# Performance work log

Measured on AMD Instinct MI355X. Metric: run time of the kernel, lower is better.

The kernel has to match this reference:

```python
import jax, jax.numpy as jnp
import numpy as np

B, N, E, ATT, TT, IT = 32, 5000, 500, 50, 4, 24
TEMP = 0.5

def leaky(x):
    return jnp.where(x > 0, x, 0.1 * x)

def ln(x, g, b, eps=1e-5):
    m = jnp.mean(x, axis=-1, keepdims=True)
    v = jnp.mean((x - m) ** 2, axis=-1, keepdims=True)
    return (x - m) * jax.lax.rsqrt(v + eps) * g + b

def setup_inputs() -> dict:
    key = jax.random.key(0)
    ks = jax.random.split(key, 16)
    s = 0.05
    return {
        'positive_sample': jax.random.randint(ks[0], (B, 3), 0, N),
        'ent_text_emb': jax.random.normal(ks[1], (N, TT, 384), jnp.float32),
        'ent_img_emb': jax.random.normal(ks[2], (N, IT, 383), jnp.float32),
        'entity_embedding': jax.random.normal(ks[3], (N, E), jnp.float32) * s,
        'relation_embedding': jax.random.normal(ks[4], (N, E), jnp.float32) * s,
        'W_text': jax.random.normal(ks[5], (ATT, 384), jnp.float32) * s,
        'b_text': jnp.zeros((ATT,), jnp.float32),
        'W_img': jax.random.normal(ks[6], (ATT, 383), jnp.float32) * s,
        'b_img': jnp.zeros((ATT,), jnp.float32),
        'W_tproj': jax.random.normal(ks[7], (ATT, ATT * IT), jnp.float32) * s,
        'b_tproj': jnp.zeros((ATT,), jnp.float32),
        'W_iproj': jax.random.normal(ks[8], (ATT, ATT * TT), jnp.float32) * s,
        'b_iproj': jnp.zeros((ATT,), jnp.float32),
        'W_rel1': jax.random.normal(ks[9], (IT * TT, E), jnp.float32) * s,
        'b_rel1': jnp.zeros((IT * TT,), jnp.float32),
        'W_rel2': jax.random.normal(ks[10], (IT * TT, E), jnp.float32) * s,
        'b_rel2': jnp.zeros((IT * TT,), jnp.float32),
        'W1': jax.random.normal(ks[11], (100, 2 * E), jnp.float32) * s,
        'b1': jnp.zeros((100,), jnp.float32),
        'W3': jax.random.normal(ks[12], (E, 100), jnp.float32) * s,
        'b3': jnp.zeros((E,), jnp.float32),
        'ln_g': jnp.ones((ATT,), jnp.float32),
        'ln_b': jnp.zeros((ATT,), jnp.float32),
    }

def _cos_sim(X, p):
    # X [B,N,d], p [B,d]; denominators are detached as in the torch code
    num = jnp.einsum('bnd,bd->bn', X, p)
    den = jnp.linalg.norm(X, axis=2) * jnp.linalg.norm(p, axis=1)[:, None]
    return num / (jax.lax.stop_gradient(den) + 1e-10)

def reference(positive_sample, ent_text_emb, ent_img_emb, entity_embedding,
              relation_embedding, W_text, b_text, W_img, b_img, W_tproj, b_tproj,
              W_iproj, b_iproj, W_rel1, b_rel1, W_rel2, b_rel2, W1, b1, W3, b3,
              ln_g, ln_b):
    rel = relation_embedding[positive_sample[:, 1]]              # [B,E]
    text_emb = leaky(jnp.einsum('ntf,df->ntd', ent_text_emb, W_text) + b_text)  # [N,4,50]
    img_emb = leaky(jnp.einsum('nif,df->nid', ent_img_emb, W_img) + b_img)      # [N,24,50]
    cross = jnp.einsum('nid,ntd->nit', img_emb, text_emb)        # [N,24,4]

    # image branch: softmax over img tokens, plus relation-gated path
    img_att = jnp.einsum('nti,nid->ntd', jax.nn.softmax(cross.transpose(0, 2, 1), axis=2), img_emb)  # [N,4,50]
    rg_i = jax.nn.sigmoid(rel @ W_rel1.T + b_rel1).reshape(B, IT, TT)           # [B,24,4]
    gated_i = rg_i[:, None] * cross[None]                                        # [B,N,24,4]
    img_att_rg = jnp.einsum('bnit,nid->bntd', gated_i, img_emb)                  # [B,N,4,50]
    img_att_all = ln(img_att_rg, ln_g, ln_b) + ln(img_att, ln_g, ln_b)[None]
    img_att_all = img_att_all.reshape(B, N, TT * ATT) @ W_iproj.T + b_iproj      # [B,N,50]

    # text branch: softmax over text tokens, plus relation-gated path
    text_att = jnp.einsum('nit,ntd->nid', jax.nn.softmax(cross, axis=2), text_emb)  # [N,24,50]
    rg_t = jax.nn.sigmoid(rel @ W_rel2.T + b_rel2).reshape(B, IT, TT)
    gated_t = rg_t[:, None] * cross[None]                                        # [B,N,24,4]
    text_att_rg = jnp.einsum('bnit,ntd->bnid', gated_t, text_emb)                # [B,N,24,50]
    text_att_all = ln(text_att_rg, ln_g, ln_b) + ln(text_att, ln_g, ln_b)[None]
    text_att_all = text_att_all.reshape(B, N, IT * ATT) @ W_tproj.T + b_tproj    # [B,N,50]

    # structural gate on KGE entity embeddings (split W1 to avoid concat)
    h = leaky(entity_embedding @ W1[:, :E].T[None].squeeze(0).T.T  # placeholder removed below
              ) if False else None
    h = leaky((entity_embedding @ W1[:, :E].T)[None] + (rel @ W1[:, E:].T)[:, None] + b1)  # [B,N,100]
    gate = jax.nn.sigmoid(h @ W3.T + b3)                                         # [B,N,E]
    t_att = entity_embedding[None] * gate                                        # [B,N,E]

    pos_idx = positive_sample[:, 2]  # tail-batch
    bi = jnp.arange(B)
    pos_img = img_att_all[bi, pos_idx]    # [B,50]
    pos_text = text_att_all[bi, pos_idx]  # [B,50]
    pos_t = t_att[bi, pos_idx]            # [B,E]

    simil_img = _cos_sim(img_att_all, pos_img)
    simil_text = _cos_sim(text_att_all, pos_text)
    simil_t = _cos_sim(t_att, pos_t)

    out = (jax.nn.softmax(simil_t / TEMP, axis=1)
           + jax.nn.softmax(simil_img / TEMP, axis=1)
           + jax.nn.softmax(simil_text / TEMP, axis=1))
    return (out, simil_img, simil_text, simil_t)
```

## Files before the change

### kernel.cpp

```cpp
#include <hip/hip_runtime.h>
#include <math.h>

#define BB 32
#define NN 5000
#define EE 500
#define AT 50
#define TTT 4
#define ITT 24
#define FT 384
#define FI 383
#define KH 100
#define BN (BB*NN)

__device__ __forceinline__ float leaky(float x){ return x > 0.f ? x : 0.1f*x; }
__device__ __forceinline__ float sigm(float x){ return 1.f/(1.f+__expf(-x)); }

enum : size_t {
  O_WTT = 0,
  O_WIT = 19968,
  O_WIP = 39936,
  O_WTP = 50336,
  O_W1T = 112736,
  O_W3T = 162736,
  O_SIP = 212736,
  O_STP = 212944,
  O_CBI = 214192,
  O_CBT = 214244,
  O_RGI = 214296,
  O_RGT = 217368,
  O_RB  = 220440,
  O_A   = 223640,
  O_PT  = 723640,
  O_PTN = 739640,
  O_PIM = 739672,
  O_PIMN= 741336,
  O_PTX = 741368,
  O_PTXN= 743032,
  O_MR  = 743064,
  O_SR  = 743160,
  O_EMB = 743256,
};

__global__ void k_prep(const float* Wt, const float* Wi, const float* Wip, const float* Wtp,
                       const float* W1, const float* W3, const float* g, const float* lb,
                       const float* bip, const float* btp, float* ws){
  (void)W1;
  int id = blockIdx.x*256 + threadIdx.x;
  if (id < 19968){ int f=id/52, d=id%52; ws[O_WTT+id] = (d<50)? Wt[d*FT+f] : 0.f; return; }
  id -= 19968;
  if (id < 19968){ int f=id/52, d=id%52; ws[O_WIT+id] = (f<383 && d<50)? Wi[d*FI+f] : 0.f; return; }
  id -= 19968;
  if (id < 10400){
    int m=id>>2, c=id&3; int d=m%50, r=m/50; int q=r%13, t=r/13; int o=q*4+c;
    ws[O_WIP+id] = (o<50)? Wip[o*200+t*50+d]*g[o] : 0.f; return; }
  id -= 10400;
  if (id < 62400){
    int m=id>>2, c=id&3; int d=m%50, r=m/50; int q=r%13, i=r/13; int o=q*4+c;
    ws[O_WTP+id] = (o<50)? Wtp[o*1200+i*50+d]*g[o] : 0.f; return; }
  id -= 62400;
  if (id < 50000){ int k=id/500, e=id%500; ws[O_W3T+id] = W3[e*100+k]; return; }
  id -= 50000;
  if (id < 208){ int t=id/52, o=id%52; float s=0;
                 if (o<50) for(int d=0;d<50;d++) s += Wip[o*200+t*50+d]*g[d];
                 ws[O_SIP+id]=s; return; }
  id -= 208;
  if (id < 1248){ int i=id/52, o=id%52; float s=0;
                  if (o<50) for(int d=0;d<50;d++) s += Wtp[o*1200+i*50+d]*g[d];
                  ws[O_STP+id]=s; return; }
  id -= 1248;
  if (id < 52){ int o=id; float s=0;
                if (o<50){ for(int j=0;j<200;j++) s += lb[j%50]*Wip[o*200+j]; s=2.f*s+bip[o]; }
                ws[O_CBI+o]=s; return; }
  id -= 52;
  if (id < 52){ int o=id; float s=0;
                if (o<50){ for(int j=0;j<1200;j++) s += lb[j%50]*Wtp[o*1200+j]; s=2.f*s+btp[o]; }
                ws[O_CBT+o]=s; return; }
}

__global__ void k_rel(const int* ps, const float* rele, const float* Wr1, const float* br1,
                      const float* Wr2, const float* br2, const float* W1, float* ws){
  __shared__ float relL[EE];
  int b = blockIdx.x;
  int r = ps[b*3+1];
  for (int e=threadIdx.x; e<EE; e+=256) relL[e] = rele[(size_t)r*EE+e];
  __syncthreads();
  for (int j=threadIdx.x; j<292; j+=256){
    if (j<96){
      float a=br1[j]; const float* w=&Wr1[j*EE];
      for(int e=0;e<EE;e++) a+=relL[e]*w[e];
      ws[O_RGI+b*96+j]=sigm(a);
    } else if (j<192){
      int jj=j-96; float a=br2[jj]; const float* w=&Wr2[jj*EE];
      for(int e=0;e<EE;e++) a+=relL[e]*w[e];
      ws[O_RGT+b*96+jj]=sigm(a);
    } else {
      int k=j-192; float a=0; const float* w=&W1[k*1000+500];
      for(int e=0;e<EE;e++) a+=relL[e]*w[e];
      ws[O_RB+b*100+k]=a;
    }
  }
}

__global__ void k_A(const float* ent, const float* W1, float* ws){
  __shared__ __align__(16) float entL[8*EE];
  int n0 = blockIdx.x*8;
  for (int idx=threadIdx.x; idx<1000; idx+=256)
    *(float4*)&entL[idx*4] = *(const float4*)&ent[(size_t)n0*EE + idx*4];
  __syncthreads();
  for (int idx=threadIdx.x; idx<800; idx+=256){
    int k=idx>>3, rr=idx&7;
    const float4* el=(const float4*)&entL[rr*EE];
    const float4* wr=(const float4*)&W1[(size_t)k*1000];
    float s=0;
    for (int e4=0;e4<125;e4++){
      float4 a=el[e4], w=wr[e4];
      s += a.x*w.x + a.y*w.y + a.z*w.z + a.w*w.w;
    }
    ws[O_A + (size_t)k*NN + (n0+rr)] = s;
  }
}

__global__ void k_pos(const int* ps, const float* ent, const float* b1, const float* b3, float* ws){
  __shared__ float hL[KH];
  __shared__ float red[4];
  int b=blockIdx.x; int n=ps[b*3+2]; int tid=threadIdx.x;
  if (tid<KH) hL[tid] = leaky(ws[O_A+(size_t)tid*NN+n] + ws[O_RB+b*100+tid] + b1[tid]);
  __syncthreads();
  const float* w3t=&ws[O_W3T];
  float sq=0;
  for (int e=tid; e<EE; e+=256){
    float a=b3[e];
    for (int k=0;k<KH;k++) a += hL[k]*w3t[k*500+e];
    float gg=sigm(a); float ta=ent[(size_t)n*EE+e]*gg;
    ws[O_PT+b*500+e]=ta; sq+=ta*ta;
  }
  for (int off=1; off<64; off<<=1) sq += __shfl_xor(sq, off);
  if ((tid&63)==0) red[tid>>6]=sq;
  __syncthreads();
  if (tid==0) ws[O_PTN+b] = sqrtf(red[0]+red[1]+red[2]+red[3]);
}

__global__ __launch_bounds__(256) void k_emb(const float* X, const float* Wp, const float* bias,
                                             float* emb, int R, int F, int rowsPerN, int rowOff,
                                             int xstride){
  __shared__ __align__(16) float Wl[128*52];
  int row0 = blockIdx.x*512 + threadIdx.x;
  int row1 = row0 + 256;
  bool act0 = row0 < R, act1 = row1 < R;
  float4 acc0[13], acc1[13];
  #pragma unroll
  for (int c=0;c<13;c++){ acc0[c]=make_float4(0,0,0,0); acc1[c]=make_float4(0,0,0,0); }
  const float* xr0 = X + (size_t)(act0?row0:0)*xstride;
  const float* xr1 = X + (size_t)(act1?row1:0)*xstride;
  for (int f0=0; f0<F; f0+=128){
    int nf = min(128, F-f0);
    __syncthreads();
    for (int j=threadIdx.x; j<nf*52; j+=256) Wl[j] = Wp[(size_t)f0*52 + j];
    __syncthreads();
    for (int f=0; f<nf; ++f){
      float x0 = xr0[f0+f], x1 = xr1[f0+f];
      const float4* wr = (const float4*)&Wl[f*52];
      #pragma unroll
      for (int c=0;c<13;++c){
        float4 w=wr[c];
        acc0[c].x+=x0*w.x; acc0[c].y+=x0*w.y; acc0[c].z+=x0*w.z; acc0[c].w+=x0*w.w;
        acc1[c].x+=x1*w.x; acc1[c].y+=x1*w.y; acc1[c].z+=x1*w.z; acc1[c].w+=x1*w.w;
      }
    }
  }
  if (act0){
    int n = row0 / rowsPerN, rr = row0 % rowsPerN;
    float* dst = emb + (size_t)n*1456 + (size_t)(rowOff+rr)*52;
    #pragma unroll
    for (int c=0;c<13;++c){
      float4 v=acc0[c]; int o=c*4;
      v.x=leaky(v.x+bias[o]); v.y=leaky(v.y+bias[o+1]);
      if (c<12){ v.z=leaky(v.z+bias[o+2]); v.w=leaky(v.w+bias[o+3]); }
      else { v.z=0.f; v.w=0.f; }
      *(float4*)&dst[o]=v;
    }
  }
  if (act1){
    int n = row1 / rowsPerN, rr = row1 % rowsPerN;
    float* dst = emb + (size_t)n*1456 + (size_t)(rowOff+rr)*52;
    #pragma unroll
    for (int c=0;c<13;++c){
      float4 v=acc1[c]; int o=c*4;
      v.x=leaky(v.x+bias[o]); v.y=leaky(v.y+bias[o+1]);
      if (c<12){ v.z=leaky(v.z+bias[o+2]); v.w=leaky(v.w+bias[o+3]); }
      else { v.z=0.f; v.w=0.f; }
      *(float4*)&dst[o]=v;
    }
  }
}

__global__ __launch_bounds__(256) void k_main(const int* ps, float* ws, float* out, int mode){
  __shared__ __align__(16) float teie[1456];
  __shared__ __align__(16) float Pm[120*52];
  __shared__ __align__(16) float Um[120*32];
  __shared__ __align__(16) float Gi[576];
  __shared__ __align__(16) float crs[96];
  __shared__ __align__(16) float aimg[96], atxt[96];
  __shared__ __align__(16) float part1[96], part2[96];
  __shared__ __align__(16) float aU[120];
  __shared__ float Gts[16], mimg[24], mtxt[4];
  __shared__ float muA1[4], muA2[24];
  __shared__ float accD1[32], accN1[32], accD2[32], accN2[32];

  int tid = threadIdx.x;
  int bstar = blockIdx.x;
  int n = mode ? ps[bstar*3+2] : blockIdx.x;

  const float* embn = &ws[O_EMB + (size_t)n*1456];
  for (int j=tid; j<364; j+=256) *(float4*)&teie[j*4] = *(const float4*)&embn[j*4];
  if (tid<32){ accD1[tid]=0.f; accN1[tid]=0.f; accD2[tid]=0.f; accN2[tid]=0.f; }
  __syncthreads();

  for (int it=tid; it<716; it+=256){
    if (it<576){
      int i=it/24, j=it%24;
      const float4* a=(const float4*)&teie[(4+i)*52];
      const float4* b=(const float4*)&teie[(4+j)*52];
      float s=0;
      #pragma unroll
      for(int d=0;d<13;d++){ float4 x=a[d], y=b[d]; s+=x.x*y.x+x.y*y.y+x.z*y.z+x.w*y.w; }
      Gi[it]=s;
    } else if (it<672){
      int c=it-576; int i=c>>2, t=c&3;
      const float4* a=(const float4*)&teie[(4+i)*52];
      const float4* b=(const float4*)&teie[t*52];
      float s=0;
      #pragma unroll
      for(int d=0;d<13;d++){ float4 x=a[d], y=b[d]; s+=x.x*y.x+x.y*y.y+x.z*y.z+x.w*y.w; }
      crs[c]=s;
    } else if (it<688){
      int c=it-672; int t=c>>2, u=c&3;
      const float4* a=(const float4*)&teie[t*52];
      const float4* b=(const float4*)&teie[u*52];
      float s=0;
      #pragma unroll
      for(int d=0;d<13;d++){ float4 x=a[d], y=b[d]; s+=x.x*y.x+x.y*y.y+x.z*y.z+x.w*y.w; }
      Gts[c]=s;
    } else if (it<712){
      int i=it-688;
      const float4* a=(const float4*)&teie[(4+i)*52];
      float s=0;
      #pragma unroll
      for(int d=0;d<13;d++){ float4 x=a[d]; s+=x.x+x.y+x.z+x.w; }
      mimg[i]=s*0.02f;
    } else {
      int t=it-712;
      const float4* a=(const float4*)&teie[t*52];
      float s=0;
      #pragma unroll
      for(int d=0;d<13;d++){ float4 x=a[d]; s+=x.x+x.y+x.z+x.w; }
      mtxt[t]=s*0.02f;
    }
  }
  __syncthreads();

  if (tid<4){
    int t=tid;
    float mx=-1e30f; for(int i=0;i<24;i++) mx=fmaxf(mx,crs[i*4+t]);
    float ex[24]; float s=0;
    for(int i=0;i<24;i++){ ex[i]=__expf(crs[i*4+t]-mx); s+=ex[i]; }
    float inv=1.f/s; float mu=0;
    for(int i=0;i<24;i++){ float a=ex[i]*inv; aimg[i*4+t]=a; mu+=a*mimg[i]; }
    muA1[t]=mu;
  } else if (tid>=64 && tid<88){
    int i=tid-64;
    float mx=-1e30f; for(int t=0;t<4;t++) mx=fmaxf(mx,crs[i*4+t]);
    float ex[4]; float s=0;
    for(int t=0;t<4;t++){ ex[t]=__expf(crs[i*4+t]-mx); s+=ex[t]; }
    float inv=1.f/s; float mu=0;
    for(int t=0;t<4;t++){ float a=ex[t]*inv; atxt[i*4+t]=a; mu+=a*mtxt[t]; }
    muA2[i]=mu;
  }
  __syncthreads();

  if (tid<208){
    int ig=tid&3, r=tid>>2, q=r%13, t=r/13;
    const float* wb = &ws[O_WIP + (size_t)(t*13+q)*200];
    const float* eb = &teie[(4+ig*6)*52];
    float4 acc[6];
    #pragma unroll
    for (int l=0;l<6;l++) acc[l]=make_float4(0,0,0,0);
    for (int dc=0; dc<12; ++dc){
      float e[6][4];
      #pragma unroll
      for (int l=0;l<6;l++){
        float4 v=*(const float4*)&eb[l*52+dc*4];
        e[l][0]=v.x; e[l][1]=v.y; e[l][2]=v.z; e[l][3]=v.w;
      }
      #pragma unroll
      for (int dd=0; dd<4; ++dd){
        float4 w=*(const float4*)&wb[(dc*4+dd)*4];
        #pragma unroll
        for (int l=0;l<6;l++){
          acc[l].x+=e[l][dd]*w.x; acc[l].y+=e[l][dd]*w.y;
          acc[l].z+=e[l][dd]*w.z; acc[l].w+=e[l][dd]*w.w;
        }
      }
    }
    #pragma unroll
    for (int d=48; d<50; ++d){
      float4 w=*(const float4*)&wb[d*4];
      #pragma unroll
      for (int l=0;l<6;l++){
        float ee=eb[l*52+d];
        acc[l].x+=ee*w.x; acc[l].y+=ee*w.y; acc[l].z+=ee*w.z; acc[l].w+=ee*w.w;
      }
    }
    #pragma unroll
    for (int l=0;l<6;l++) *(float4*)&Pm[(t*24+ig*6+l)*52 + q*4]=acc[l];
  } else {
    for (int c=tid-208; c<244; c+=48){
      if (c<96){
        int i=c>>2, t=c&3;
        float s=0; for(int j=0;j<24;j++) s+=Gi[i*24+j]*aimg[j*4+t];
        part1[c]=aimg[c]*s;
      } else if (c<192){
        int cc=c-96; int t=cc&3;
        float s=0; for(int u=0;u<4;u++) s+=Gts[t*4+u]*atxt[(cc&~3)+u];
        part2[cc]=atxt[cc]*s;
      } else {
        int j=c-192;
        *(float4*)&Pm[96*52+j*4] = *(const float4*)&ws[O_SIP+j*4];
      }
    }
  }
  __syncthreads();

  if (tid<128){
    int b=tid&31, t=tid>>5;
    float w1r[24];
    #pragma unroll
    for(int i=0;i<24;i++) w1r[i]=ws[O_RGI+b*96+i*4+t]*crs[i*4+t];
    float mu=0;
    #pragma unroll
    for(int i=0;i<24;i++) mu+=w1r[i]*mimg[i];
    float q=0;
    #pragma unroll
    for(int i=0;i<24;i++){
      const float4* gr=(const float4*)&Gi[i*24];
      float s=0;
      #pragma unroll
      for(int j4=0;j4<6;j4++){
        float4 g=gr[j4];
        s+=g.x*w1r[j4*4]+g.y*w1r[j4*4+1]+g.z*w1r[j4*4+2]+g.w*w1r[j4*4+3];
      }
      q+=w1r[i]*s;
    }
    float inv=rsqrtf(q*0.02f-mu*mu+1e-5f);
    #pragma unroll
    for(int i=0;i<24;i++) Um[(t*24+i)*32+b]=inv*w1r[i];
    Um[(96+t)*32+b]=-inv*mu;
  } else if (tid<228){
    int z=tid-128;
    int t=(z<96)? (z/24) : (z-96);
    float q=0; for(int i=0;i<24;i++) q+=part1[i*4+t];
    float inv=rsqrtf(q*0.02f-muA1[t]*muA1[t]+1e-5f);
    aU[z]=(z<96)? inv*aimg[(z%24)*4+t] : -inv*muA1[t];
  }
  __syncthreads();

  if (tid<104){
    int bg=tid/13, q=tid-bg*13;
    float4 a0=make_float4(0,0,0,0), a1=make_float4(0,0,0,0);
    float4 a2=make_float4(0,0,0,0), a3=make_float4(0,0,0,0);
    for (int z=0; z<100; ++z){
      float az=aU[z];
      float4 u=*(const float4*)&Um[z*32+bg*4];
      float4 p=*(const float4*)&Pm[z*52+q*4];
      float u0=u.x+az, u1=u.y+az, u2=u.z+az, u3=u.w+az;
      a0.x+=u0*p.x; a0.y+=u0*p.y; a0.z+=u0*p.z; a0.w+=u0*p.w;
      a1.x+=u1*p.x; a1.y+=u1*p.y; a1.z+=u1*p.z; a1.w+=u1*p.w;
      a2.x+=u2*p.x; a2.y+=u2*p.y; a2.z+=u2*p.z; a2.w+=u2*p.w;
      a3.x+=u3*p.x; a3.y+=u3*p.y; a3.z+=u3*p.z; a3.w+=u3*p.w;
    }
    float4 cb=*(const float4*)&ws[O_CBI+q*4];
    a0.x+=cb.x; a0.y+=cb.y; a0.z+=cb.z; a0.w+=cb.w;
    a1.x+=cb.x; a1.y+=cb.y; a1.z+=cb.z; a1.w+=cb.w;
    a2.x+=cb.x; a2.y+=cb.y; a2.z+=cb.z; a2.w+=cb.w;
    a3.x+=cb.x; a3.y+=cb.y; a3.z+=cb.z; a3.w+=cb.w;
    float n0=a0.x*a0.x+a0.y*a0.y+a0.z*a0.z+a0.w*a0.w;
    float n1=a1.x*a1.x+a1.y*a1.y+a1.z*a1.z+a1.w*a1.w;
    float n2=a2.x*a2.x+a2.y*a2.y+a2.z*a2.z+a2.w*a2.w;
    float n3=a3.x*a3.x+a3.y*a3.y+a3.z*a3.z+a3.w*a3.w;
    int b0=bg*4;
    if (!mode){
      const float* PV=&ws[O_PIM];
      float4 p0=*(const float4*)&PV[(b0+0)*52+q*4];
      float4 p1=*(const float4*)&PV[(b0+1)*52+q*4];
      float4 p2=*(const float4*)&PV[(b0+2)*52+q*4];
      float4 p3=*(const float4*)&PV[(b0+3)*52+q*4];
      atomicAdd(&accD1[b0+0], a0.x*p0.x+a0.y*p0.y+a0.z*p0.z+a0.w*p0.w);
      atomicAdd(&accD1[b0+1], a1.x*p1.x+a1.y*p1.y+a1.z*p1.z+a1.w*p1.w);
      atomicAdd(&accD1[b0+2], a2.x*p2.x+a2.y*p2.y+a2.z*p2.z+a2.w*p2.w);
      atomicAdd(&accD1[b0+3], a3.x*p3.x+a3.y*p3.y+a3.z*p3.z+a3.w*p3.w);
      atomicAdd(&accN1[b0+0],n0); atomicAdd(&accN1[b0+1],n1);
      atomicAdd(&accN1[b0+2],n2); atomicAdd(&accN1[b0+3],n3);
    } else {
      atomicAdd(&accN1[b0+0],n0); atomicAdd(&accN1[b0+1],n1);
      atomicAdd(&accN1[b0+2],n2); atomicAdd(&accN1[b0+3],n3);
      if ((bstar>>2)==bg){
        int bl=bstar&3;
        float4 sel = (bl==0)? a0 : (bl==1)? a1 : (bl==2)? a2 : a3;
        *(float4*)&ws[O_PIM+(size_t)bstar*52+q*4]=sel;
      }
    }
  }
  __syncthreads();

  if (!mode){
    if (tid<32)
      out[(size_t)BN + (size_t)tid*NN + n] = accD1[tid]/(sqrtf(accN1[tid])*ws[O_PIMN+tid]+1e-10f);
  } else {
    if (tid==0) ws[O_PIMN+bstar]=sqrtf(accN1[bstar]);
  }
  if (tid<156){
    int q=tid%13, i2=tid/13;
    const float* wbA = &ws[O_WTP + (size_t)((i2*2+0)*13+q)*200];
    const float* wbB = &ws[O_WTP + (size_t)((i2*2+1)*13+q)*200];
    float4 accA[4], accB[4];
    #pragma unroll
    for (int t=0;t<4;t++){ accA[t]=make_float4(0,0,0,0); accB[t]=make_float4(0,0,0,0); }
    for (int dc=0; dc<12; ++dc){
      float e[4][4];
      #pragma unroll
      for (int t=0;t<4;t++){
        float4 v=*(const float4*)&teie[t*52+dc*4];
        e[t][0]=v.x; e[t][1]=v.y; e[t][2]=v.z; e[t][3]=v.w;
      }
      #pragma unroll
      for (int dd=0; dd<4; ++dd){
        float4 wA=*(const float4*)&wbA[(dc*4+dd)*4];
        float4 wB=*(const float4*)&wbB[(dc*4+dd)*4];
        #pragma unroll
        for (int t=0;t<4;t++){
          accA[t].x+=e[t][dd]*wA.x; accA[t].y+=e[t][dd]*wA.y;
          accA[t].z+=e[t][dd]*wA.z; accA[t].w+=e[t][dd]*wA.w;
          accB[t].x+=e[t][dd]*wB.x; accB[t].y+=e[t][dd]*wB.y;
          accB[t].z+=e[t][dd]*wB.z; accB[t].w+=e[t][dd]*wB.w;
        }
      }
    }
    #pragma unroll
    for (int d=48; d<50; ++d){
      float4 wA=*(const float4*)&wbA[d*4];
      float4 wB=*(const float4*)&wbB[d*4];
      #pragma unroll
      for (int t=0;t<4;t++){
        float ee=teie[t*52+d];
        accA[t].x+=ee*wA.x; accA[t].y+=ee*wA.y; accA[t].z+=ee*wA.z; accA[t].w+=ee*wA.w;
        accB[t].x+=ee*wB.x; accB[t].y+=ee*wB.y; accB[t].z+=ee*wB.z; accB[t].w+=ee*wB.w;
      }
    }
    #pragma unroll
    for (int t=0;t<4;t++){
      *(float4*)&Pm[(t*24+i2*2+0)*52 + q*4]=accA[t];
      *(float4*)&Pm[(t*24+i2*2+1)*52 + q*4]=accB[t];
    }
  } else {
    for (int j=tid-156; j<312; j+=100)
      *(float4*)&Pm[96*52+j*4] = *(const float4*)&ws[O_STP+j*4];
  }
  __syncthreads();

  for (int it=tid; it<888; it+=256){
    if (it<768){
      int b=it&31, i=it>>5;
      float w2r[4];
      #pragma unroll
      for(int t=0;t<4;t++) w2r[t]=ws[O_RGT+b*96+i*4+t]*crs[i*4+t];
      float mu=0;
      #pragma unroll
      for(int t=0;t<4;t++) mu+=w2r[t]*mtxt[t];
      float q=0;
      #pragma unroll
      for(int t=0;t<4;t++){
        float s=0;
        #pragma unroll
        for(int u=0;u<4;u++) s+=Gts[t*4+u]*w2r[u];
        q+=w2r[t]*s;
      }
      float inv=rsqrtf(q*0.02f-mu*mu+1e-5f);
      #pragma unroll
      for(int t=0;t<4;t++) Um[(t*24+i)*32+b]=inv*w2r[t];
      Um[(96+i)*32+b]=-inv*mu;
    } else {
      int z=it-768;
      int i=(z<96)? (z%24) : (z-96);
      float q=0; for(int t=0;t<4;t++) q+=part2[i*4+t];
      float inv=rsqrtf(q*0.02f-muA2[i]*muA2[i]+1e-5f);
      aU[z]=(z<96)? inv*atxt[(z%24)*4+(z/24)] : -inv*muA2[i];
    }
  }
  __syncthreads();

  if (tid<104){
    int bg=tid/13, q=tid-bg*13;
    float4 a0=make_float4(0,0,0,0), a1=make_float4(0,0,0,0);
    float4 a2=make_float4(0,0,0,0), a3=make_float4(0,0,0,0);
    for (int z=0; z<120; ++z){
      float az=aU[z];
      float4 u=*(const float4*)&Um[z*32+bg*4];
      float4 p=*(const float4*)&Pm[z*52+q*4];
      float u0=u.x+az, u1=u.y+az, u2=u.z+az, u3=u.w+az;
      a0.x+=u0*p.x; a0.y+=u0*p.y; a0.z+=u0*p.z; a0.w+=u0*p.w;
      a1.x+=u1*p.x; a1.y+=u1*p.y; a1.z+=u1*p.z; a1.w+=u1*p.w;
      a2.x+=u2*p.x; a2.y+=u2*p.y; a2.z+=u2*p.z; a2.w+=u2*p.w;
      a3.x+=u3*p.x; a3.y+=u3*p.y; a3.z+=u3*p.z; a3.w+=u3*p.w;
    }
    float4 cb=*(const float4*)&ws[O_CBT+q*4];
    a0.x+=cb.x; a0.y+=cb.y; a0.z+=cb.z; a0.w+=cb.w;
    a1.x+=cb.x; a1.y+=cb.y; a1.z+=cb.z; a1.w+=cb.w;
    a2.x+=cb.x; a2.y+=cb.y; a2.z+=cb.z; a2.w+=cb.w;
    a3.x+=cb.x; a3.y+=cb.y; a3.z+=cb.z; a3.w+=cb.w;
    float n0=a0.x*a0.x+a0.y*a0.y+a0.z*a0.z+a0.w*a0.w;
    float n1=a1.x*a1.x+a1.y*a1.y+a1.z*a1.z+a1.w*a1.w;
    float n2=a2.x*a2.x+a2.y*a2.y+a2.z*a2.z+a2.w*a2.w;
    float n3=a3.x*a3.x+a3.y*a3.y+a3.z*a3.z+a3.w*a3.w;
    int b0=bg*4;
    if (!mode){
      const float* PV=&ws[O_PTX];
      float4 p0=*(const float4*)&PV[(b0+0)*52+q*4];
      float4 p1=*(const float4*)&PV[(b0+1)*52+q*4];
      float4 p2=*(const float4*)&PV[(b0+2)*52+q*4];
      float4 p3=*(const float4*)&PV[(b0+3)*52+q*4];
      atomicAdd(&accD2[b0+0], a0.x*p0.x+a0.y*p0.y+a0.z*p0.z+a0.w*p0.w);
      atomicAdd(&accD2[b0+1], a1.x*p1.x+a1.y*p1.y+a1.z*p1.z+a1.w*p1.w);
      atomicAdd(&accD2[b0+2], a2.x*p2.x+a2.y*p2.y+a2.z*p2.z+a2.w*p2.w);
      atomicAdd(&accD2[b0+3], a3.x*p3.x+a3.y*p3.y+a3.z*p3.z+a3.w*p3.w);
      atomicAdd(&accN2[b0+0],n0); atomicAdd(&accN2[b0+1],n1);
      atomicAdd(&accN2[b0+2],n2); atomicAdd(&accN2[b0+3],n3);
    } else {
      atomicAdd(&accN2[b0+0],n0); atomicAdd(&accN2[b0+1],n1);
      atomicAdd(&accN2[b0+2],n2); atomicAdd(&accN2[b0+3],n3);
      if ((bstar>>2)==bg){
        int bl=bstar&3;
        float4 sel = (bl==0)? a0 : (bl==1)? a1 : (bl==2)? a2 : a3;
        *(float4*)&ws[O_PTX+(size_t)bstar*52+q*4]=sel;
      }
    }
  }
  __syncthreads();

  if (!mode){
    if (tid<32)
      out[2*(size_t)BN + (size_t)tid*NN + n] = accD2[tid]/(sqrtf(accN2[tid])*ws[O_PTXN+tid]+1e-10f);
  } else {
    if (tid==0) ws[O_PTXN+bstar]=sqrtf(accN2[bstar]);
  }
}

__global__ __launch_bounds__(256) void k_gate(const float* ent, const float* b1, const float* b3,
                                              float* ws, float* out){
  __shared__ __align__(16) float hL[50*68];
  __shared__ __align__(16) float wc[50*128];
  __shared__ __align__(16) float PTb[512];
  __shared__ __align__(16) float b3L[512];
  __shared__ float rbL[KH];

  int tid = threadIdx.x;
  int b   = blockIdx.x & 31;
  int n0  = (blockIdx.x >> 5) * 64;

  for (int j=tid; j<512; j+=256){
    PTb[j] = (j<EE)? ws[O_PT + b*EE + j] : 0.f;
    b3L[j] = (j<EE)? b3[j] : 0.f;
  }
  if (tid < KH) rbL[tid] = ws[O_RB + b*KH + tid] + b1[tid];

  int ej = tid & 31;
  int ni = tid >> 5;

  float pn[8], ps[8];
  #pragma unroll
  for (int r=0;r<8;r++){ pn[r]=0.f; ps[r]=0.f; }

  for (int ec=0; ec<4; ++ec){
    int e0 = ec*128;
    float4 acc[8];
    #pragma unroll
    for (int r=0;r<8;r++) acc[r]=make_float4(0,0,0,0);

    for (int kh=0; kh<2; ++kh){
      __syncthreads();
      for (int idx=tid; idx<1600; idx+=256){
        int k = idx>>5, j4 = idx&31;
        int e = e0 + j4*4;
        float4 v = make_float4(0,0,0,0);
        if (e+3 < EE) v = *(const float4*)&ws[O_W3T + (size_t)(kh*50+k)*EE + e];
        *(float4*)&wc[k*128 + j4*4] = v;
      }
      for (int idx=tid; idx<3200; idx+=256){
        int k = idx>>6, nn = idx&63;
        int n = n0 + nn;
        float v = 0.f;
        if (n < NN) v = leaky(ws[O_A + (size_t)(kh*50+k)*NN + n] + rbL[kh*50+k]);
        hL[k*68 + nn] = v;
      }
      __syncthreads();

      const float4* wp = (const float4*)&wc[ej*4];
      const float4* hp = (const float4*)&hL[ni*8];
      #pragma unroll 2
      for (int k=0;k<50;k++){
        float4 w  = wp[k*32];
        float4 h0 = hp[k*17];
        float4 h1 = hp[k*17 + 1];
        acc[0].x+=h0.x*w.x; acc[0].y+=h0.x*w.y; acc[0].z+=h0.x*w.z; acc[0].w+=h0.x*w.w;
        acc[1].x+=h0.y*w.x; acc[1].y+=h0.y*w.y; acc[1].z+=h0.y*w.z; acc[1].w+=h0.y*w.w;
        acc[2].x+=h0.z*w.x; acc[2].y+=h0.z*w.y; acc[2].z+=h0.z*w.z; acc[2].w+=h0.z*w.w;
        acc[3].x+=h0.w*w.x; acc[3].y+=h0.w*w.y; acc[3].z+=h0.w*w.z; acc[3].w+=h0.w*w.w;
        acc[4].x+=h1.x*w.x; acc[4].y+=h1.x*w.y; acc[4].z+=h1.x*w.z; acc[4].w+=h1.x*w.w;
        acc[5].x+=h1.y*w.x; acc[5].y+=h1.y*w.y; acc[5].z+=h1.y*w.z; acc[5].w+=h1.y*w.w;
        acc[6].x+=h1.z*w.x; acc[6].y+=h1.z*w.y; acc[6].z+=h1.z*w.z; acc[6].w+=h1.z*w.w;
        acc[7].x+=h1.w*w.x; acc[7].y+=h1.w*w.y; acc[7].z+=h1.w*w.z; acc[7].w+=h1.w*w.w;
      }
    }

    {
      int ebase = e0 + ej*4;
      bool ev = (ebase + 3) < EE;
      float4 bb = *(const float4*)&b3L[ebase];
      float4 pt = *(const float4*)&PTb[ebase];
      #pragma unroll
      for (int r=0;r<8;r++){
        int n = n0 + ni*8 + r;
        float4 en = make_float4(0,0,0,0);
        if (ev && n < NN) en = *(const float4*)&ent[(size_t)n*EE + ebase];
        float t0 = en.x * sigm(acc[r].x + bb.x);
        float t1 = en.y * sigm(acc[r].y + bb.y);
        float t2 = en.z * sigm(acc[r].z + bb.z);
        float t3 = en.w * sigm(acc[r].w + bb.w);
        pn[r] += t0*pt.x + t1*pt.y + t2*pt.z + t3*pt.w;
        ps[r] += t0*t0 + t1*t1 + t2*t2 + t3*t3;
      }
    }
  }

  for (int off=1; off<32; off<<=1){
    #pragma unroll
    for (int r=0;r<8;r++){ pn[r]+=__shfl_xor(pn[r],off); ps[r]+=__shfl_xor(ps[r],off); }
  }
  if (ej==0){
    float ptn = ws[O_PTN+b];
    #pragma unroll
    for (int r=0;r<8;r++){
      int n = n0 + ni*8 + r;
      if (n < NN)
        out[3*(size_t)BN + (size_t)b*NN + n] = pn[r]/(sqrtf(ps[r])*ptn + 1e-10f);
    }
  }
}

__global__ void k_smax1(const float* out, float* ws){
  __shared__ float red[4];
  __shared__ float Msh;
  int a=blockIdx.x>>5, b=blockIdx.x&31, tid=threadIdx.x;
  const float* arr=&out[(size_t)(1+a)*BN + (size_t)b*NN];
  float mx=-1e30f;
  for (int i=tid;i<NN;i+=256) mx=fmaxf(mx,arr[i]);
  for (int off=1;off<64;off<<=1) mx=fmaxf(mx,__shfl_xor(mx,off));
  if ((tid&63)==0) red[tid>>6]=mx;
  __syncthreads();
  if (tid==0) Msh=fmaxf(fmaxf(red[0],red[1]),fmaxf(red[2],red[3]));
  __syncthreads();
  float M2=2.f*Msh;
  float s=0;
  for (int i=tid;i<NN;i+=256) s+=__expf(2.f*arr[i]-M2);
  for (int off=1;off<64;off<<=1) s+=__shfl_xor(s,off);
  if ((tid&63)==0) red[tid>>6]=s;
  __syncthreads();
  if (tid==0){ ws[O_MR+a*32+b]=M2; ws[O_SR+a*32+b]=red[0]+red[1]+red[2]+red[3]; }
}

__global__ void k_smax2(float* out, const float* ws){
  int t=blockIdx.x*256+threadIdx.x;
  if (t>=BN) return;
  int b=t/NN;
  float r=0;
  for (int a=0;a<3;a++)
    r += __expf(2.f*out[(size_t)(1+a)*BN+t]-ws[O_MR+a*32+b])/ws[O_SR+a*32+b];
  out[t]=r;
}

extern "C" void kernel_launch(void* const* d_in, const int* in_sizes, int n_in,
                              void* d_out, int out_size, void* d_ws, size_t ws_size,
                              hipStream_t stream){
  (void)in_sizes; (void)n_in; (void)out_size; (void)ws_size;
  const int*   ps  =(const int*)  d_in[0];
  const float* etg =(const float*)d_in[1];
  const float* eig =(const float*)d_in[2];
  const float* ent =(const float*)d_in[3];
  const float* rele=(const float*)d_in[4];
  const float* Wt  =(const float*)d_in[5];
  const float* btx =(const float*)d_in[6];
  const float* Wi  =(const float*)d_in[7];
  const float* bim =(const float*)d_in[8];
  const float* Wtp =(const float*)d_in[9];
  const float* btp =(const float*)d_in[10];
  const float* Wip =(const float*)d_in[11];
  const float* bip =(const float*)d_in[12];
  const float* Wr1 =(const float*)d_in[13];
  const float* br1 =(const float*)d_in[14];
  const float* Wr2 =(const float*)d_in[15];
  const float* br2 =(const float*)d_in[16];
  const float* W1  =(const float*)d_in[17];
  const float* b1  =(const float*)d_in[18];
  const float* W3  =(const float*)d_in[19];
  const float* b3  =(const float*)d_in[20];
  const float* lng =(const float*)d_in[21];
  const float* lnb =(const float*)d_in[22];
  float* ws =(float*)d_ws;
  float* out=(float*)d_out;

  k_prep <<<642,256,0,stream>>>(Wt,Wi,Wip,Wtp,W1,W3,lng,lnb,bip,btp,ws);
  k_rel  <<<32, 256,0,stream>>>(ps,rele,Wr1,br1,Wr2,br2,W1,ws);
  k_A    <<<625,256,0,stream>>>(ent,W1,ws);
  k_pos  <<<32, 256,0,stream>>>(ps,ent,b1,b3,ws);
  k_emb  <<<40, 256,0,stream>>>(etg,&ws[O_WTT],btx,&ws[O_EMB],20000,FT,4,0,FT);
  k_emb  <<<235,256,0,stream>>>(eig,&ws[O_WIT],bim,&ws[O_EMB],120000,FI,24,4,FI);
  k_main <<<32,  256,0,stream>>>(ps,ws,out,1);
  k_main <<<5000,256,0,stream>>>(ps,ws,out,0);
  k_gate <<<32*79,256,0,stream>>>(ent,b1,b3,ws,out);
  k_smax1<<<96, 256,0,stream>>>(out,ws);
  k_smax2<<<625,256,0,stream>>>(out,ws);
}
```

Measured before the change: 1.666 ms.

## Split embedding projection over feature chunks with atomic accumulation

Replaces the single embedding projection kernel, which ran with very few blocks, with three steps: bias init, a split-K accumulation kernel that divides the 384/383 features into four chunks and atomically adds partial sums, and a final leaky-ReLU pass. This adds more blocks so the GPU is better filled, where before only 40 and 235 blocks ran. In exchange, weights are read from global memory instead of LDS, the atomics add traffic and make results order-dependent, and two extra launches and passes over the buffer are added.

Result: slower. 3.225 ms (+93.6%).

```diff
diff --git a/kernel.cpp b/kernel.cpp
--- a/kernel.cpp
+++ b/kernel.cpp
@@ -140,57 +140,64 @@
   if (tid==0) ws[O_PTN+b] = sqrtf(red[0]+red[1]+red[2]+red[3]);
 }
 
-__global__ __launch_bounds__(256) void k_emb(const float* X, const float* Wp, const float* bias,
-                                             float* emb, int R, int F, int rowsPerN, int rowOff,
-                                             int xstride){
-  __shared__ __align__(16) float Wl[128*52];
-  int row0 = blockIdx.x*512 + threadIdx.x;
-  int row1 = row0 + 256;
-  bool act0 = row0 < R, act1 = row1 < R;
-  float4 acc0[13], acc1[13];
+__global__ void k_emb_bias(const float* bias, float* emb, int R, int rowsPerN, int rowOff){
+  int row = blockIdx.x*256 + threadIdx.x;
+  if (row >= R) return;
+  int n = row / rowsPerN, rr = row % rowsPerN;
+  float* dst = emb + (size_t)n*1456 + (size_t)(rowOff+rr)*52;
   #pragma unroll
-  for (int c=0;c<13;c++){ acc0[c]=make_float4(0,0,0,0); acc1[c]=make_float4(0,0,0,0); }
-  const float* xr0 = X + (size_t)(act0?row0:0)*xstride;
-  const float* xr1 = X + (size_t)(act1?row1:0)*xstride;
-  for (int f0=0; f0<F; f0+=128){
-    int nf = min(128, F-f0);
-    __syncthreads();
-    for (int j=threadIdx.x; j<nf*52; j+=256) Wl[j] = Wp[(size_t)f0*52 + j];
-    __syncthreads();
-    for (int f=0; f<nf; ++f){
-      float x0 = xr0[f0+f], x1 = xr1[f0+f];
-      const float4* wr = (const float4*)&Wl[f*52];
-      #pragma unroll
-      for (int c=0;c<13;++c){
-        float4 w=wr[c];
-        acc0[c].x+=x0*w.x; acc0[c].y+=x0*w.y; acc0[c].z+=x0*w.z; acc0[c].w+=x0*w.w;
-        acc1[c].x+=x1*w.x; acc1[c].y+=x1*w.y; acc1[c].z+=x1*w.z; acc1[c].w+=x1*w.w;
-      }
-    }
-  }
-  if (act0){
-    int n = row0 / rowsPerN, rr = row0 % rowsPerN;
-    float* dst = emb + (size_t)n*1456 + (size_t)(rowOff+rr)*52;
+  for (int c=0;c<13;c++){
+    float4 v;
+    v.x = bias[c*4+0];
+    v.y = bias[c*4+1];
+    v.z = (c<12)? bias[c*4+2] : 0.f;
+    v.w = (c<12)? bias[c*4+3] : 0.f;
+    *(float4*)&dst[c*4] = v;
+  }
+}
+
+__global__ __launch_bounds__(256) void k_emb_acc(const float* X, const float* Wp,
+                                                 float* emb, int R, int F, int rowsPerN,
+                                                 int rowOff, int xstride){
+  int rb = blockIdx.x >> 2, ch = blockIdx.x & 3;
+  int row = rb*256 + threadIdx.x;
+  if (row >= R) return;
+  int f0 = ch*96;
+  int nf = min(96, F - f0);
+  const float* xr = X + (size_t)row*xstride + f0;
+  const float4* wp = (const float4*)&Wp[(size_t)f0*52];
+  float4 acc[13];
+  #pragma unroll
+  for (int c=0;c<13;c++) acc[c]=make_float4(0,0,0,0);
+  for (int f=0; f<nf; ++f){
+    float x = xr[f];
+    const float4* wr = wp + (size_t)f*13;
     #pragma unroll
     for (int c=0;c<13;++c){
-      float4 v=acc0[c]; int o=c*4;
-      v.x=leaky(v.x+bias[o]); v.y=leaky(v.y+bias[o+1]);
-      if (c<12){ v.z=leaky(v.z+bias[o+2]); v.w=leaky(v.w+bias[o+3]); }
-      else { v.z=0.f; v.w=0.f; }
-      *(float4*)&dst[o]=v;
-    }
-  }
-  if (act1){
-    int n = row1 / rowsPerN, rr = row1 % rowsPerN;
-    float* dst = emb + (size_t)n*1456 + (size_t)(rowOff+rr)*52;
-    #pragma unroll
-    for (int c=0;c<13;++c){
-      float4 v=acc1[c]; int o=c*4;
-      v.x=leaky(v.x+bias[o]); v.y=leaky(v.y+bias[o+1]);
-      if (c<12){ v.z=leaky(v.z+bias[o+2]); v.w=leaky(v.w+bias[o+3]); }
-      else { v.z=0.f; v.w=0.f; }
-      *(float4*)&dst[o]=v;
-    }
+      float4 w=wr[c];
+      acc[c].x+=x*w.x; acc[c].y+=x*w.y; acc[c].z+=x*w.z; acc[c].w+=x*w.w;
+    }
+  }
+  int n = row / rowsPerN, rr = row % rowsPerN;
+  float* dst = emb + (size_t)n*1456 + (size_t)(rowOff+rr)*52;
+  #pragma unroll
+  for (int c=0;c<12;c++){
+    atomicAdd(&dst[c*4+0], acc[c].x);
+    atomicAdd(&dst[c*4+1], acc[c].y);
+    atomicAdd(&dst[c*4+2], acc[c].z);
+    atomicAdd(&dst[c*4+3], acc[c].w);
+  }
+  atomicAdd(&dst[48], acc[12].x);
+  atomicAdd(&dst[49], acc[12].y);
+}
+
+__global__ void k_emb_fin(float* emb, int total4){
+  int idx = blockIdx.x*256 + threadIdx.x;
+  int stride = gridDim.x*256;
+  for (int i=idx; i<total4; i+=stride){
+    float4 v = *(float4*)&emb[(size_t)i*4];
+    v.x=leaky(v.x); v.y=leaky(v.y); v.z=leaky(v.z); v.w=leaky(v.w);
+    *(float4*)&emb[(size_t)i*4]=v;
   }
 }
 
@@ -721,8 +728,11 @@
   k_rel  <<<32, 256,0,stream>>>(ps,rele,Wr1,br1,Wr2,br2,W1,ws);
   k_A    <<<625,256,0,stream>>>(ent,W1,ws);
   k_pos  <<<32, 256,0,stream>>>(ps,ent,b1,b3,ws);
-  k_emb  <<<40, 256,0,stream>>>(etg,&ws[O_WTT],btx,&ws[O_EMB],20000,FT,4,0,FT);
-  k_emb  <<<235,256,0,stream>>>(eig,&ws[O_WIT],bim,&ws[O_EMB],120000,FI,24,4,FI);
+  k_emb_bias<<<79, 256,0,stream>>>(btx,&ws[O_EMB],20000,4,0);
+  k_emb_bias<<<469,256,0,stream>>>(bim,&ws[O_EMB],120000,24,4);
+  k_emb_acc <<<79*4, 256,0,stream>>>(etg,&ws[O_WTT],&ws[O_EMB],20000,FT,4,0,FT);
+  k_emb_acc <<<469*4,256,0,stream>>>(eig,&ws[O_WIT],&ws[O_EMB],120000,FI,24,4,FI);
+  k_emb_fin <<<2048,256,0,stream>>>(&ws[O_EMB],1820000);
   k_main <<<32,  256,0,stream>>>(ps,ws,out,1);
   k_main <<<5000,256,0,stream>>>(ps,ws,out,0);
   k_gate <<<32*79,256,0,stream>>>(ent,b1,b3,ws,out);
```

## Split embedding projection over feature dimension across warps with shared reduction

Applied to the files above, without the earlier changes.

Rewrites the embedding projection kernel so each block handles 64 rows, with its four wavefronts each covering a quarter of the feature dimension. Partial sums are combined through shared memory. This raises the block count from 40/235 to 313/1875 to fill the GPU better. Weights are now read directly from global memory (wave-uniform, cache-friendly) instead of being staged in LDS, which trades extra cache traffic and a reduction step for more parallelism.

Result: faster. 1.457 ms (-12.6%).

```diff
diff --git a/kernel.cpp b/kernel.cpp
--- a/kernel.cpp
+++ b/kernel.cpp
@@ -140,56 +140,53 @@
   if (tid==0) ws[O_PTN+b] = sqrtf(red[0]+red[1]+red[2]+red[3]);
 }
 
-__global__ __launch_bounds__(256) void k_emb(const float* X, const float* Wp, const float* bias,
-                                             float* emb, int R, int F, int rowsPerN, int rowOff,
-                                             int xstride){
-  __shared__ __align__(16) float Wl[128*52];
-  int row0 = blockIdx.x*512 + threadIdx.x;
-  int row1 = row0 + 256;
-  bool act0 = row0 < R, act1 = row1 < R;
-  float4 acc0[13], acc1[13];
+__global__ __launch_bounds__(256) void k_emb2(const float* __restrict__ X,
+                                              const float* __restrict__ Wp,
+                                              const float* __restrict__ bias,
+                                              float* __restrict__ emb,
+                                              int R, int F, int rowsPerN, int rowOff,
+                                              int xstride){
+  __shared__ __align__(16) float part[4][64][52];
+  int tid = threadIdx.x;
+  int lane = tid & 63;
+  int w = __builtin_amdgcn_readfirstlane(tid >> 6);
+  int row = blockIdx.x*64 + lane;
+  int fq = (F + 3) >> 2;
+  int f0 = w*fq;
+  int f1 = min(F, f0+fq);
+  float4 acc[13];
   #pragma unroll
-  for (int c=0;c<13;c++){ acc0[c]=make_float4(0,0,0,0); acc1[c]=make_float4(0,0,0,0); }
-  const float* xr0 = X + (size_t)(act0?row0:0)*xstride;
-  const float* xr1 = X + (size_t)(act1?row1:0)*xstride;
-  for (int f0=0; f0<F; f0+=128){
-    int nf = min(128, F-f0);
-    __syncthreads();
-    for (int j=threadIdx.x; j<nf*52; j+=256) Wl[j] = Wp[(size_t)f0*52 + j];
-    __syncthreads();
-    for (int f=0; f<nf; ++f){
-      float x0 = xr0[f0+f], x1 = xr1[f0+f];
-      const float4* wr = (const float4*)&Wl[f*52];
+  for (int c=0;c<13;c++) acc[c]=make_float4(0,0,0,0);
+  if (row < R){
+    const float* xr = X + (size_t)row*xstride;
+    for (int f=f0; f<f1; ++f){
+      float x = xr[f];
+      const float4* wr = (const float4*)(Wp + (size_t)f*52);
       #pragma unroll
       for (int c=0;c<13;++c){
-        float4 w=wr[c];
-        acc0[c].x+=x0*w.x; acc0[c].y+=x0*w.y; acc0[c].z+=x0*w.z; acc0[c].w+=x0*w.w;
-        acc1[c].x+=x1*w.x; acc1[c].y+=x1*w.y; acc1[c].z+=x1*w.z; acc1[c].w+=x1*w.w;
-      }
-    }
-  }
-  if (act0){
-    int n = row0 / rowsPerN, rr = row0 % rowsPerN;
-    float* dst = emb + (size_t)n*1456 + (size_t)(rowOff+rr)*52;
-    #pragma unroll
-    for (int c=0;c<13;++c){
-      float4 v=acc0[c]; int o=c*4;
-      v.x=leaky(v.x+bias[o]); v.y=leaky(v.y+bias[o+1]);
-      if (c<12){ v.z=leaky(v.z+bias[o+2]); v.w=leaky(v.w+bias[o+3]); }
-      else { v.z=0.f; v.w=0.f; }
-      *(float4*)&dst[o]=v;
-    }
-  }
-  if (act1){
-    int n = row1 / rowsPerN, rr = row1 % rowsPerN;
-    float* dst = emb + (size_t)n*1456 + (size_t)(rowOff+rr)*52;
-    #pragma unroll
-    for (int c=0;c<13;++c){
-      float4 v=acc1[c]; int o=c*4;
-      v.x=leaky(v.x+bias[o]); v.y=leaky(v.y+bias[o+1]);
-      if (c<12){ v.z=leaky(v.z+bias[o+2]); v.w=leaky(v.w+bias[o+3]); }
-      else { v.z=0.f; v.w=0.f; }
-      *(float4*)&dst[o]=v;
+        float4 wv=wr[c];
+        acc[c].x+=x*wv.x; acc[c].y+=x*wv.y; acc[c].z+=x*wv.z; acc[c].w+=x*wv.w;
+      }
+    }
+  }
+  #pragma unroll
+  for (int c=0;c<13;c++) *(float4*)&part[w][lane][c*4] = acc[c];
+  __syncthreads();
+  for (int g=tid; g<832; g+=256){
+    int r = g/13, q = g-r*13;
+    int row2 = blockIdx.x*64 + r;
+    if (row2 < R){
+      float4 s0 = *(const float4*)&part[0][r][q*4];
+      float4 s1 = *(const float4*)&part[1][r][q*4];
+      float4 s2 = *(const float4*)&part[2][r][q*4];
+      float4 s3 = *(const float4*)&part[3][r][q*4];
+      float4 v;
+      v.x = leaky(s0.x+s1.x+s2.x+s3.x + bias[q*4+0]);
+      v.y = leaky(s0.y+s1.y+s2.y+s3.y + bias[q*4+1]);
+      v.z = (q<12)? leaky(s0.z+s1.z+s2.z+s3.z + bias[q*4+2]) : 0.f;
+      v.w = (q<12)? leaky(s0.w+s1.w+s2.w+s3.w + bias[q*4+3]) : 0.f;
+      int n = row2 / rowsPerN, rr = row2 % rowsPerN;
+      *(float4*)&emb[(size_t)n*1456 + (size_t)(rowOff+rr)*52 + q*4] = v;
     }
   }
 }
@@ -721,8 +718,8 @@
   k_rel  <<<32, 256,0,stream>>>(ps,rele,Wr1,br1,Wr2,br2,W1,ws);
   k_A    <<<625,256,0,stream>>>(ent,W1,ws);
   k_pos  <<<32, 256,0,stream>>>(ps,ent,b1,b3,ws);
-  k_emb  <<<40, 256,0,stream>>>(etg,&ws[O_WTT],btx,&ws[O_EMB],20000,FT,4,0,FT);
-  k_emb  <<<235,256,0,stream>>>(eig,&ws[O_WIT],bim,&ws[O_EMB],120000,FI,24,4,FI);
+  k_emb2 <<<313, 256,0,stream>>>(etg,&ws[O_WTT],btx,&ws[O_EMB],20000,FT,4,0,FT);
+  k_emb2 <<<1875,256,0,stream>>>(eig,&ws[O_WIT],bim,&ws[O_EMB],120000,FI,24,4,FI);
   k_main <<<32,  256,0,stream>>>(ps,ws,out,1);
   k_main <<<5000,256,0,stream>>>(ps,ws,out,0);
   k_gate <<<32*79,256,0,stream>>>(ent,b1,b3,ws,out);
```
